# Performance work log

Measured on AMD Instinct MI355X. Metric: run time of the kernel, lower is better.

Reference implementation:

```python
import jax, jax.numpy as jnp
import numpy as np

EPS = 1e-7  # K.epsilon()


def setup_inputs() -> dict:
    key = jax.random.key(0)
    k1, k2, k3, k4 = jax.random.split(key, 4)
    B, T, D = 64, 1024, 256
    x = jax.random.normal(k1, (B, T, D), dtype=jnp.float32)
    # keras initializers.get('normal') -> RandomNormal(stddev=0.05)
    W = jax.random.normal(k2, (D, T), dtype=jnp.float32) * 0.05
    b = jax.random.normal(k3, (T,), dtype=jnp.float32) * 0.05
    u = jax.random.normal(k4, (T, 1), dtype=jnp.float32) * 0.05
    mask = jnp.ones((B, T), dtype=bool)
    return {"x": x, "W": W, "b": b, "u": u, "mask": mask}


def reference(x, W, b, u, mask):
    # x: [B,T,D], W: [D,T] -> uit: [B,T,T]
    uit = jnp.tanh(jnp.einsum('btd,dk->btk', x, W) + b)
    ait = jnp.einsum('btk,ko->bt', uit, u)          # [B,T]
    ait = jnp.exp(ait)
    ait = ait * mask.astype(x.dtype)
    ait = ait / (jnp.sum(ait, axis=1, keepdims=True) + EPS)
    return jnp.einsum('btd,bt->bd', x, ait)         # [B,D]
```

## Files before the change

kernel.cpp:

```cpp
#include <hip/hip_runtime.h>
#include <hip/hip_bf16.h>
#include <cstdint>

#define EPS 1e-7f

typedef __attribute__((ext_vector_type(8))) short short8;
typedef __attribute__((ext_vector_type(4))) float f32x4;

union bf8u { unsigned short u[8]; short8 v; };

static __device__ __forceinline__ unsigned short f2bf(float f) {
    unsigned int u = __builtin_bit_cast(unsigned int, f);
    unsigned int r = (u + 0x7fffu + ((u >> 16) & 1u)) >> 16;
    return (unsigned short)r;
}

static __device__ __forceinline__ void gload_lds16(const void* g, void* l) {
    __builtin_amdgcn_global_load_lds((const __attribute__((address_space(1))) void*)g,
                                     (__attribute__((address_space(3))) void*)l,
                                     16, 0, 0);
}

__global__ void k_transpose(const float* __restrict__ W, unsigned short* __restrict__ Wt) {
    __shared__ float tile[64][65];
    int j0 = blockIdx.x * 64;
    int d0 = blockIdx.y * 64;
    int tr = threadIdx.x >> 6;
    int tc = threadIdx.x & 63;
    #pragma unroll
    for (int i = 0; i < 16; ++i) {
        int dr = i * 4 + tr;
        tile[dr][tc] = W[(d0 + dr) * 1024 + j0 + tc];
    }
    __syncthreads();
    #pragma unroll
    for (int i = 0; i < 16; ++i) {
        int jr = i * 4 + tr;
        Wt[(size_t)(j0 + jr) * 256 + d0 + tc] = f2bf(tile[tc][jr]);
    }
}

__global__ void __launch_bounds__(256, 2)
k_logits(const float* __restrict__ x,
         const unsigned short* __restrict__ Wt,
         const float* __restrict__ bvec,
         const float* __restrict__ uvec,
         float* __restrict__ lp) {
    __shared__ unsigned char lds[65536];

    const int tid = threadIdx.x;
    const int m0 = blockIdx.x * 128;
    const int wv = tid >> 6, l = tid & 63, lr = l & 15, lg = l >> 4;

    {
        #pragma unroll
        for (int i = 0; i < 8; ++i) {
            int f16i = tid + i * 256;
            int jr = f16i >> 5, c16 = f16i & 31;
            int srcoff = (c16 * 16) ^ ((jr & 7) << 4);
            gload_lds16((const unsigned char*)(Wt + (size_t)jr * 256) + srcoff,
                        lds + f16i * 16);
        }
    }

    short8 afrag[2][8];
    {
        const float* xw = x + ((size_t)m0 + wv * 32 + lr) * 256 + lg * 8;
        #pragma unroll
        for (int r = 0; r < 2; ++r) {
            const float* xr = xw + (size_t)r * 16 * 256;
            #pragma unroll
            for (int kk = 0; kk < 8; ++kk) {
                float4 v0 = *(const float4*)(xr + kk * 32);
                float4 v1 = *(const float4*)(xr + kk * 32 + 4);
                bf8u a;
                a.u[0] = f2bf(v0.x); a.u[1] = f2bf(v0.y);
                a.u[2] = f2bf(v0.z); a.u[3] = f2bf(v0.w);
                a.u[4] = f2bf(v1.x); a.u[5] = f2bf(v1.y);
                a.u[6] = f2bf(v1.z); a.u[7] = f2bf(v1.w);
                afrag[r][kk] = a.v;
            }
        }
    }

    float negp[2][4];
    #pragma unroll
    for (int r = 0; r < 2; ++r)
        #pragma unroll
        for (int i = 0; i < 4; ++i) negp[r][i] = 0.f;
    float usum = 0.f;

    const float C = 2.88539008177793f;

    __syncthreads();

    for (int c = 0; c < 16; ++c) {
        if (c < 15) {
            unsigned char* nb = lds + ((c + 1) & 1) * 32768;
            int j0n = (c + 1) * 64;
            #pragma unroll
            for (int i = 0; i < 8; ++i) {
                int f16i = tid + i * 256;
                int jr = f16i >> 5, c16 = f16i & 31;
                int srcoff = (c16 * 16) ^ ((jr & 7) << 4);
                gload_lds16((const unsigned char*)(Wt + (size_t)(j0n + jr) * 256) + srcoff,
                            nb + f16i * 16);
            }
        }
        const unsigned char* buf = lds + (c & 1) * 32768;
        int j0 = c * 64;

        #pragma unroll
        for (int jt = 0; jt < 4; ++jt) {
            int jrow = jt * 16 + lr;
            int rowbase = jrow * 512;
            int sw = (jrow & 7) << 4;
            f32x4 a0 = {0.f, 0.f, 0.f, 0.f}, a1 = a0;
            #pragma unroll
            for (int kk = 0; kk < 8; ++kk) {
                short8 bf = *(const short8*)(buf + rowbase + ((kk * 64 + lg * 16) ^ sw));
                a0 = __builtin_amdgcn_mfma_f32_16x16x32_bf16(afrag[0][kk], bf, a0, 0, 0, 0);
                a1 = __builtin_amdgcn_mfma_f32_16x16x32_bf16(afrag[1][kk], bf, a1, 0, 0, 0);
            }
            float bb = bvec[j0 + jt * 16 + lr];
            float uj = uvec[j0 + jt * 16 + lr];
            float bbC = bb * C;
            usum += uj;
            #pragma unroll
            for (int i = 0; i < 4; ++i) {
                float e0 = exp2f(fmaf(a0[i], C, bbC));
                negp[0][i] = fmaf(uj, __builtin_amdgcn_rcpf(e0 + 1.f), negp[0][i]);
                float e1 = exp2f(fmaf(a1[i], C, bbC));
                negp[1][i] = fmaf(uj, __builtin_amdgcn_rcpf(e1 + 1.f), negp[1][i]);
            }
        }
        __syncthreads();
    }

    #pragma unroll
    for (int off = 8; off; off >>= 1) {
        usum += __shfl_xor(usum, off, 16);
        #pragma unroll
        for (int r = 0; r < 2; ++r)
            #pragma unroll
            for (int i = 0; i < 4; ++i)
                negp[r][i] += __shfl_xor(negp[r][i], off, 16);
    }
    if (lr == 0) {
        float* o = lp + m0 + wv * 32 + lg * 4;
        #pragma unroll
        for (int r = 0; r < 2; ++r)
            #pragma unroll
            for (int i = 0; i < 4; ++i)
                o[r * 16 + i] = usum - 2.f * negp[r][i];
    }
}

__global__ void k_softmax(const float* __restrict__ lp, float* __restrict__ wts) {
    __shared__ float red[256];
    int b = blockIdx.x;
    int tid = threadIdx.x;
    const float* lg = lp + b * 1024;
    float e0 = __expf(lg[tid]);
    float e1 = __expf(lg[tid + 256]);
    float e2 = __expf(lg[tid + 512]);
    float e3 = __expf(lg[tid + 768]);
    red[tid] = e0 + e1 + e2 + e3;
    __syncthreads();
    for (int off = 128; off; off >>= 1) {
        if (tid < off) red[tid] += red[tid + off];
        __syncthreads();
    }
    float inv = __fdividef(1.0f, red[0] + EPS);
    float* wb = wts + b * 1024;
    wb[tid]       = e0 * inv;
    wb[tid + 256] = e1 * inv;
    wb[tid + 512] = e2 * inv;
    wb[tid + 768] = e3 * inv;
}

__global__ void k_wsum(const float* __restrict__ x, const float* __restrict__ wts,
                       float* __restrict__ partials) {
    int chunk = blockIdx.x;
    int b = blockIdx.y;
    int d = threadIdx.x;
    const float* xb = x + ((size_t)b * 1024 + chunk * 64) * 256;
    const float* wb = wts + b * 1024 + chunk * 64;
    float acc = 0.f;
    #pragma unroll 4
    for (int t = 0; t < 64; ++t)
        acc += xb[t * 256 + d] * wb[t];
    partials[((size_t)chunk * 64 + b) * 256 + d] = acc;
}

__global__ void k_reduce(const float* __restrict__ partials, float* __restrict__ out) {
    int idx = blockIdx.x * 256 + threadIdx.x;
    float acc = 0.f;
    #pragma unroll
    for (int c = 0; c < 16; ++c)
        acc += partials[c * 16384 + idx];
    out[idx] = acc;
}

extern "C" void kernel_launch(void* const* d_in, const int* in_sizes, int n_in,
                              void* d_out, int out_size, void* d_ws, size_t ws_size,
                              hipStream_t stream) {
    const float* x = (const float*)d_in[0];
    const float* W = (const float*)d_in[1];
    const float* b = (const float*)d_in[2];
    const float* u = (const float*)d_in[3];
    float* out = (float*)d_out;

    unsigned char* ws = (unsigned char*)d_ws;
    unsigned short* Wt = (unsigned short*)ws;
    float* lp       = (float*)(ws + 524288);
    float* partials = (float*)(ws + 524288);
    float* wts      = (float*)(ws + 1572864);

    hipLaunchKernelGGL(k_transpose, dim3(16, 4), dim3(256), 0, stream, W, Wt);
    hipLaunchKernelGGL(k_logits, dim3(512), dim3(256), 0, stream, x, Wt, b, u, lp);
    hipLaunchKernelGGL(k_softmax, dim3(64), dim3(256), 0, stream, lp, wts);
    hipLaunchKernelGGL(k_wsum, dim3(16, 64), dim3(256), 0, stream, x, wts, partials);
    hipLaunchKernelGGL(k_reduce, dim3(64), dim3(256), 0, stream, partials, out);
}
```

Measured before the change: 77.99 us.

## Restructure logits kernel: 512-thread blocks, smaller W chunks, manual vmcnt pipelining

```diff
diff --git a/kernel.cpp b/kernel.cpp
--- a/kernel.cpp
+++ b/kernel.cpp
@@ -20,6 +20,8 @@
                                      (__attribute__((address_space(3))) void*)l,
                                      16, 0, 0);
 }
+
+#define SB() __builtin_amdgcn_sched_barrier(0)
 
 __global__ void k_transpose(const float* __restrict__ W, unsigned short* __restrict__ Wt) {
     __shared__ float tile[64][65];
@@ -40,27 +42,39 @@
     }
 }
 
-__global__ void __launch_bounds__(256, 2)
+__global__ void __launch_bounds__(512, 2)
 k_logits(const float* __restrict__ x,
          const unsigned short* __restrict__ Wt,
          const float* __restrict__ bvec,
          const float* __restrict__ uvec,
          float* __restrict__ lp) {
-    __shared__ unsigned char lds[65536];
+    __shared__ unsigned char lds[40960];
 
     const int tid = threadIdx.x;
-    const int m0 = blockIdx.x * 128;
+    const int m0 = blockIdx.x * 256;
     const int wv = tid >> 6, l = tid & 63, lr = l & 15, lg = l >> 4;
-
-    {
-        #pragma unroll
-        for (int i = 0; i < 8; ++i) {
-            int f16i = tid + i * 256;
-            int jr = f16i >> 5, c16 = f16i & 31;
-            int srcoff = (c16 * 16) ^ ((jr & 7) << 4);
-            gload_lds16((const unsigned char*)(Wt + (size_t)jr * 256) + srcoff,
-                        lds + f16i * 16);
-        }
+    const float C = 2.88539008177793f;
+
+    int sof[2], dof[2];
+    #pragma unroll
+    for (int i = 0; i < 2; ++i) {
+        int f16i = tid + i * 512;
+        int jr = f16i >> 5, c16 = f16i & 31;
+        sof[i] = jr * 512 + ((c16 * 16) ^ ((jr & 7) << 4));
+        dof[i] = f16i * 16;
+    }
+
+    #pragma unroll
+    for (int i = 0; i < 2; ++i)
+        gload_lds16((const unsigned char*)Wt + sof[i], lds + dof[i]);
+
+    #pragma unroll
+    for (int t = 0; t < 2; ++t) {
+        int j = tid + t * 512;
+        float2 v;
+        v.x = bvec[j] * C;
+        v.y = uvec[j];
+        *(float2*)(lds + 32768 + j * 8) = v;
     }
 
     short8 afrag[2][8];
@@ -90,51 +104,54 @@
         for (int i = 0; i < 4; ++i) negp[r][i] = 0.f;
     float usum = 0.f;
 
-    const float C = 2.88539008177793f;
-
     __syncthreads();
 
-    for (int c = 0; c < 16; ++c) {
-        if (c < 15) {
-            unsigned char* nb = lds + ((c + 1) & 1) * 32768;
-            int j0n = (c + 1) * 64;
-            #pragma unroll
-            for (int i = 0; i < 8; ++i) {
-                int f16i = tid + i * 256;
-                int jr = f16i >> 5, c16 = f16i & 31;
-                int srcoff = (c16 * 16) ^ ((jr & 7) << 4);
-                gload_lds16((const unsigned char*)(Wt + (size_t)(j0n + jr) * 256) + srcoff,
-                            nb + f16i * 16);
-            }
+    for (int c = 0; c < 32; ++c) {
+        if (c < 31) {
+            unsigned char* nb = lds + ((c + 1) & 1) * 16384;
+            const unsigned char* src = (const unsigned char*)Wt + (size_t)(c + 1) * 16384;
+            #pragma unroll
+            for (int i = 0; i < 2; ++i)
+                gload_lds16(src + sof[i], nb + dof[i]);
+            SB();
+            asm volatile("s_waitcnt vmcnt(2)" ::: "memory");
+        } else {
+            SB();
+            asm volatile("s_waitcnt vmcnt(0)" ::: "memory");
         }
-        const unsigned char* buf = lds + (c & 1) * 32768;
-        int j0 = c * 64;
-
-        #pragma unroll
-        for (int jt = 0; jt < 4; ++jt) {
+        __builtin_amdgcn_s_barrier();
+        SB();
+
+        const unsigned char* buf = lds + (c & 1) * 16384;
+        const int j0 = c * 32;
+
+        #pragma unroll
+        for (int jt = 0; jt < 2; ++jt) {
             int jrow = jt * 16 + lr;
             int rowbase = jrow * 512;
             int sw = (jrow & 7) << 4;
+            float2 bu = *(const float2*)(lds + 32768 + (size_t)(j0 + jrow) * 8);
             f32x4 a0 = {0.f, 0.f, 0.f, 0.f}, a1 = a0;
+            __builtin_amdgcn_s_setprio(1);
             #pragma unroll
             for (int kk = 0; kk < 8; ++kk) {
                 short8 bf = *(const short8*)(buf + rowbase + ((kk * 64 + lg * 16) ^ sw));
                 a0 = __builtin_amdgcn_mfma_f32_16x16x32_bf16(afrag[0][kk], bf, a0, 0, 0, 0);
                 a1 = __builtin_amdgcn_mfma_f32_16x16x32_bf16(afrag[1][kk], bf, a1, 0, 0, 0);
             }
-            float bb = bvec[j0 + jt * 16 + lr];
-            float uj = uvec[j0 + jt * 16 + lr];
-            float bbC = bb * C;
+            __builtin_amdgcn_s_setprio(0);
+            float uj = bu.y;
             usum += uj;
             #pragma unroll
             for (int i = 0; i < 4; ++i) {
-                float e0 = exp2f(fmaf(a0[i], C, bbC));
+                float e0 = exp2f(fmaf(a0[i], C, bu.x));
                 negp[0][i] = fmaf(uj, __builtin_amdgcn_rcpf(e0 + 1.f), negp[0][i]);
-                float e1 = exp2f(fmaf(a1[i], C, bbC));
+                float e1 = exp2f(fmaf(a1[i], C, bu.x));
                 negp[1][i] = fmaf(uj, __builtin_amdgcn_rcpf(e1 + 1.f), negp[1][i]);
             }
         }
-        __syncthreads();
+        SB();
+        __builtin_amdgcn_s_barrier();
     }
 
     #pragma unroll
@@ -218,7 +235,7 @@
     float* wts      = (float*)(ws + 1572864);
 
     hipLaunchKernelGGL(k_transpose, dim3(16, 4), dim3(256), 0, stream, W, Wt);
-    hipLaunchKernelGGL(k_logits, dim3(512), dim3(256), 0, stream, x, Wt, b, u, lp);
+    hipLaunchKernelGGL(k_logits, dim3(256), dim3(512), 0, stream, x, Wt, b, u, lp);
     hipLaunchKernelGGL(k_softmax, dim3(64), dim3(256), 0, stream, lp, wts);
     hipLaunchKernelGGL(k_wsum, dim3(16, 64), dim3(256), 0, stream, x, wts, partials);
     hipLaunchKernelGGL(k_reduce, dim3(64), dim3(256), 0, stream, partials, out);
```

New measurement: 88.18 us. 13.1% more time.

## Split logits over W column slices resident in LDS, sum partial logits in softmax

Applied to the files above, without the earlier changes.

```diff
diff --git a/kernel.cpp b/kernel.cpp
--- a/kernel.cpp
+++ b/kernel.cpp
@@ -40,119 +40,117 @@
     }
 }
 
-__global__ void __launch_bounds__(256, 2)
+#define BU_OFF 131072
+__global__ void __launch_bounds__(1024, 4)
 k_logits(const float* __restrict__ x,
          const unsigned short* __restrict__ Wt,
          const float* __restrict__ bvec,
          const float* __restrict__ uvec,
          float* __restrict__ lp) {
-    __shared__ unsigned char lds[65536];
+    extern __shared__ unsigned char lds[];
 
     const int tid = threadIdx.x;
-    const int m0 = blockIdx.x * 128;
-    const int wv = tid >> 6, l = tid & 63, lr = l & 15, lg = l >> 4;
+    const int p = blockIdx.x;
+    const int slice = (p >> 3) & 3;
+    const int rg = (p & 7) * 8 + (p >> 5);
+    const float C = 2.88539008177793f;
 
     {
+        const unsigned char* wsl = (const unsigned char*)(Wt + (size_t)slice * 256 * 256);
         #pragma unroll
         for (int i = 0; i < 8; ++i) {
-            int f16i = tid + i * 256;
+            int f16i = tid + i * 1024;
             int jr = f16i >> 5, c16 = f16i & 31;
-            int srcoff = (c16 * 16) ^ ((jr & 7) << 4);
-            gload_lds16((const unsigned char*)(Wt + (size_t)jr * 256) + srcoff,
-                        lds + f16i * 16);
-        }
-    }
-
-    short8 afrag[2][8];
-    {
-        const float* xw = x + ((size_t)m0 + wv * 32 + lr) * 256 + lg * 8;
+            int srcoff = jr * 512 + ((c16 * 16) ^ ((jr & 7) << 4));
+            gload_lds16(wsl + srcoff, lds + f16i * 16);
+        }
+    }
+    if (tid < 256) {
+        int jg = slice * 256 + tid;
+        float2 v;
+        v.x = bvec[jg] * C;
+        v.y = uvec[jg];
+        *(float2*)(lds + BU_OFF + tid * 8) = v;
+    }
+
+    const int wv = tid >> 6, l = tid & 63, lr = l & 15, lg = l >> 4;
+
+    __syncthreads();
+
+    #pragma unroll 1
+    for (int it = 0; it < 2; ++it) {
+        const int mbase = rg * 1024 + it * 512 + wv * 32;
+
+        short8 afrag[2][8];
+        {
+            const float* xw = x + ((size_t)mbase + lr) * 256 + lg * 8;
+            #pragma unroll
+            for (int r = 0; r < 2; ++r) {
+                const float* xr = xw + (size_t)r * 16 * 256;
+                #pragma unroll
+                for (int kk = 0; kk < 8; ++kk) {
+                    float4 v0 = *(const float4*)(xr + kk * 32);
+                    float4 v1 = *(const float4*)(xr + kk * 32 + 4);
+                    bf8u a;
+                    a.u[0] = f2bf(v0.x); a.u[1] = f2bf(v0.y);
+                    a.u[2] = f2bf(v0.z); a.u[3] = f2bf(v0.w);
+                    a.u[4] = f2bf(v1.x); a.u[5] = f2bf(v1.y);
+                    a.u[6] = f2bf(v1.z); a.u[7] = f2bf(v1.w);
+                    afrag[r][kk] = a.v;
+                }
+            }
+        }
+
+        float negp[2][4];
         #pragma unroll
-        for (int r = 0; r < 2; ++r) {
-            const float* xr = xw + (size_t)r * 16 * 256;
-            #pragma unroll
-            for (int kk = 0; kk < 8; ++kk) {
-                float4 v0 = *(const float4*)(xr + kk * 32);
-                float4 v1 = *(const float4*)(xr + kk * 32 + 4);
-                bf8u a;
-                a.u[0] = f2bf(v0.x); a.u[1] = f2bf(v0.y);
-                a.u[2] = f2bf(v0.z); a.u[3] = f2bf(v0.w);
-                a.u[4] = f2bf(v1.x); a.u[5] = f2bf(v1.y);
-                a.u[6] = f2bf(v1.z); a.u[7] = f2bf(v1.w);
-                afrag[r][kk] = a.v;
-            }
-        }
-    }
-
-    float negp[2][4];
-    #pragma unroll
-    for (int r = 0; r < 2; ++r)
-        #pragma unroll
-        for (int i = 0; i < 4; ++i) negp[r][i] = 0.f;
-    float usum = 0.f;
-
-    const float C = 2.88539008177793f;
-
-    __syncthreads();
-
-    for (int c = 0; c < 16; ++c) {
-        if (c < 15) {
-            unsigned char* nb = lds + ((c + 1) & 1) * 32768;
-            int j0n = (c + 1) * 64;
-            #pragma unroll
-            for (int i = 0; i < 8; ++i) {
-                int f16i = tid + i * 256;
-                int jr = f16i >> 5, c16 = f16i & 31;
-                int srcoff = (c16 * 16) ^ ((jr & 7) << 4);
-                gload_lds16((const unsigned char*)(Wt + (size_t)(j0n + jr) * 256) + srcoff,
-                            nb + f16i * 16);
-            }
-        }
-        const unsigned char* buf = lds + (c & 1) * 32768;
-        int j0 = c * 64;
-
-        #pragma unroll
-        for (int jt = 0; jt < 4; ++jt) {
+        for (int r = 0; r < 2; ++r)
+            #pragma unroll
+            for (int i = 0; i < 4; ++i) negp[r][i] = 0.f;
+        float usum = 0.f;
+
+        #pragma unroll 2
+        for (int jt = 0; jt < 16; ++jt) {
             int jrow = jt * 16 + lr;
             int rowbase = jrow * 512;
             int sw = (jrow & 7) << 4;
+            float2 bu = *(const float2*)(lds + BU_OFF + (size_t)jrow * 8);
             f32x4 a0 = {0.f, 0.f, 0.f, 0.f}, a1 = a0;
+            __builtin_amdgcn_s_setprio(1);
             #pragma unroll
             for (int kk = 0; kk < 8; ++kk) {
-                short8 bf = *(const short8*)(buf + rowbase + ((kk * 64 + lg * 16) ^ sw));
+                short8 bf = *(const short8*)(lds + rowbase + ((kk * 64 + lg * 16) ^ sw));
                 a0 = __builtin_amdgcn_mfma_f32_16x16x32_bf16(afrag[0][kk], bf, a0, 0, 0, 0);
                 a1 = __builtin_amdgcn_mfma_f32_16x16x32_bf16(afrag[1][kk], bf, a1, 0, 0, 0);
             }
-            float bb = bvec[j0 + jt * 16 + lr];
-            float uj = uvec[j0 + jt * 16 + lr];
-            float bbC = bb * C;
+            __builtin_amdgcn_s_setprio(0);
+            float uj = bu.y;
             usum += uj;
             #pragma unroll
             for (int i = 0; i < 4; ++i) {
-                float e0 = exp2f(fmaf(a0[i], C, bbC));
+                float e0 = exp2f(fmaf(a0[i], C, bu.x));
                 negp[0][i] = fmaf(uj, __builtin_amdgcn_rcpf(e0 + 1.f), negp[0][i]);
-                float e1 = exp2f(fmaf(a1[i], C, bbC));
+                float e1 = exp2f(fmaf(a1[i], C, bu.x));
                 negp[1][i] = fmaf(uj, __builtin_amdgcn_rcpf(e1 + 1.f), negp[1][i]);
             }
         }
-        __syncthreads();
-    }
-
-    #pragma unroll
-    for (int off = 8; off; off >>= 1) {
-        usum += __shfl_xor(usum, off, 16);
+
         #pragma unroll
-        for (int r = 0; r < 2; ++r)
-            #pragma unroll
-            for (int i = 0; i < 4; ++i)
-                negp[r][i] += __shfl_xor(negp[r][i], off, 16);
-    }
-    if (lr == 0) {
-        float* o = lp + m0 + wv * 32 + lg * 4;
-        #pragma unroll
-        for (int r = 0; r < 2; ++r)
-            #pragma unroll
-            for (int i = 0; i < 4; ++i)
-                o[r * 16 + i] = usum - 2.f * negp[r][i];
+        for (int off = 8; off; off >>= 1) {
+            usum += __shfl_xor(usum, off, 16);
+            #pragma unroll
+            for (int r = 0; r < 2; ++r)
+                #pragma unroll
+                for (int i = 0; i < 4; ++i)
+                    negp[r][i] += __shfl_xor(negp[r][i], off, 16);
+        }
+        if (lr == 0) {
+            float* o = lp + (size_t)slice * 65536 + mbase + lg * 4;
+            #pragma unroll
+            for (int r = 0; r < 2; ++r)
+                #pragma unroll
+                for (int i = 0; i < 4; ++i)
+                    o[r * 16 + i] = usum - 2.f * negp[r][i];
+        }
     }
 }
 
@@ -160,12 +158,15 @@
     __shared__ float red[256];
     int b = blockIdx.x;
     int tid = threadIdx.x;
-    const float* lg = lp + b * 1024;
-    float e0 = __expf(lg[tid]);
-    float e1 = __expf(lg[tid + 256]);
-    float e2 = __expf(lg[tid + 512]);
-    float e3 = __expf(lg[tid + 768]);
-    red[tid] = e0 + e1 + e2 + e3;
+    const float* l0 = lp + b * 1024;
+    float e[4];
+    #pragma unroll
+    for (int q = 0; q < 4; ++q) {
+        int t = tid + q * 256;
+        float s = l0[t] + l0[t + 65536] + l0[t + 131072] + l0[t + 196608];
+        e[q] = __expf(s);
+    }
+    red[tid] = e[0] + e[1] + e[2] + e[3];
     __syncthreads();
     for (int off = 128; off; off >>= 1) {
         if (tid < off) red[tid] += red[tid + off];
@@ -173,10 +174,9 @@
     }
     float inv = __fdividef(1.0f, red[0] + EPS);
     float* wb = wts + b * 1024;
-    wb[tid]       = e0 * inv;
-    wb[tid + 256] = e1 * inv;
-    wb[tid + 512] = e2 * inv;
-    wb[tid + 768] = e3 * inv;
+    #pragma unroll
+    for (int q = 0; q < 4; ++q)
+        wb[tid + q * 256] = e[q] * inv;
 }
 
 __global__ void k_wsum(const float* __restrict__ x, const float* __restrict__ wts,
@@ -217,8 +217,11 @@
     float* partials = (float*)(ws + 524288);
     float* wts      = (float*)(ws + 1572864);
 
+    hipFuncSetAttribute((const void*)k_logits,
+                        hipFuncAttributeMaxDynamicSharedMemorySize, 133120);
+
     hipLaunchKernelGGL(k_transpose, dim3(16, 4), dim3(256), 0, stream, W, Wt);
-    hipLaunchKernelGGL(k_logits, dim3(512), dim3(256), 0, stream, x, Wt, b, u, lp);
+    hipLaunchKernelGGL(k_logits, dim3(256), dim3(1024), 133120, stream, x, Wt, b, u, lp);
     hipLaunchKernelGGL(k_softmax, dim3(64), dim3(256), 0, stream, lp, wts);
     hipLaunchKernelGGL(k_wsum, dim3(16, 64), dim3(256), 0, stream, x, wts, partials);
     hipLaunchKernelGGL(k_reduce, dim3(64), dim3(256), 0, stream, partials, out);
```

Measured after the change: 89.45 us. 1.15x slower.
